# Performance work log

Measured on AMD Instinct MI355X. Metric: run time of the kernel, lower is better.

## Reference

```python
import jax, jax.numpy as jnp
import numpy as np

B, T, C = 2, 2048, 2048
HK, HV, DK, DV, KW = 16, 32, 128, 128, 4
KEY_DIM = HK * DK          # 2048
VAL_DIM = HV * DV          # 4096
QKV_DIM = 2 * KEY_DIM + VAL_DIM  # 8192
REPEAT = HV // HK
EPS = 1e-6


def setup_inputs() -> dict:
    key = jax.random.key(0)
    ks = jax.random.split(key, 12)
    s = 0.02
    return {
        "x": jax.random.normal(ks[0], (B, T, C), jnp.float32),
        "positions": jnp.arange(B * T, dtype=jnp.int64).reshape(B, T) % T,
        "W_qkv": jax.random.normal(ks[1], (QKV_DIM, C), jnp.float32) * s,
        "W_z": jax.random.normal(ks[2], (VAL_DIM, C), jnp.float32) * s,
        "W_b": jax.random.normal(ks[3], (HV, C), jnp.float32) * s,
        "W_a": jax.random.normal(ks[4], (HV, C), jnp.float32) * s,
        "conv_w": jax.random.normal(ks[5], (QKV_DIM, 1, KW), jnp.float32) * 0.3,
        "dt_bias": jnp.ones((HV,), jnp.float32),
        "A_log": jnp.log(jax.random.uniform(ks[6], (HV,), jnp.float32, 0.01, 16.0)),
        "norm_w": jnp.ones((DV,), jnp.float32),
        "W_out": jax.random.normal(ks[7], (C, VAL_DIM), jnp.float32) * s,
    }


def _forward(x, W_qkv, W_z, W_b, W_a, conv_w, dt_bias, A_log, norm_w, W_out):
    qkv = x @ W_qkv.T                                # [B,T,QKV_DIM]
    z = (x @ W_z.T).reshape(B, T, HV, DV)
    b = x @ W_b.T                                    # [B,T,HV]
    a = x @ W_a.T                                    # [B,T,HV]

    # depthwise causal conv1d (left pad KW-1), then SiLU
    qkv_c = jnp.transpose(qkv, (0, 2, 1))            # [B,QKV_DIM,T]
    qkv_c = jax.lax.conv_general_dilated(
        qkv_c, conv_w, window_strides=(1,), padding=[(KW - 1, 0)],
        dimension_numbers=("NCH", "OIH", "NCH"), feature_group_count=QKV_DIM)
    qkv = jax.nn.silu(jnp.transpose(qkv_c, (0, 2, 1)))

    q, k, v = jnp.split(qkv, [KEY_DIM, 2 * KEY_DIM], axis=-1)
    q = q.reshape(B, T, HK, DK)
    k = k.reshape(B, T, HK, DK)
    v = v.reshape(B, T, HV, DV)
    q = q / jnp.maximum(jnp.linalg.norm(q, axis=-1, keepdims=True), 1e-12)
    k = k / jnp.maximum(jnp.linalg.norm(k, axis=-1, keepdims=True), 1e-12)
    if REPEAT > 1:
        q = jnp.repeat(q, REPEAT, axis=2)            # [B,T,HV,DK]
        k = jnp.repeat(k, REPEAT, axis=2)

    beta = jax.nn.sigmoid(b)                         # [B,T,HV]
    g = -jnp.exp(A_log) * jax.nn.softplus(a + dt_bias)  # [B,T,HV]

    # gated delta-rule recurrence over time (lax.scan, time-major)
    def step(state, inp):
        g_t, beta_t, k_t, v_t, q_t = inp             # [B,HV], [B,HV], [B,HV,DK], [B,HV,DV], [B,HV,DK]
        state = jnp.exp(g_t)[..., None, None] * state \
            + beta_t[..., None, None] * (k_t[..., :, None] * v_t[..., None, :])
        out_t = jnp.einsum("bhk,bhkv->bhv", q_t, state)
        return state, out_t

    tm = lambda u: jnp.moveaxis(u, 1, 0)
    state0 = jnp.zeros((B, HV, DK, DV), x.dtype)
    _, out = jax.lax.scan(step, state0, (tm(g), tm(beta), tm(k), tm(v), tm(q)))
    out = jnp.moveaxis(out, 0, 1)                    # [B,T,HV,DV]

    # gated RMSNorm per head: RMSNorm(out) * silu(z)
    o = out.astype(jnp.float32)
    o = o * jax.lax.rsqrt(jnp.mean(o * o, axis=-1, keepdims=True) + EPS)
    o = (norm_w * o) * jax.nn.silu(z.astype(jnp.float32))
    o = o.astype(x.dtype).reshape(B, T, VAL_DIM)
    return o @ W_out.T                               # [B,T,C]


def reference(x, positions, W_qkv, W_z, W_b, W_a, conv_w, dt_bias, A_log, norm_w, W_out):
    del positions  # unused by the module's math
    return _forward(x, W_qkv, W_z, W_b, W_a, conv_w, dt_bias, A_log, norm_w, W_out)
```

## Files before the change

### kernel.cpp

```cpp
#include <hip/hip_runtime.h>

typedef unsigned short u16;
typedef unsigned int u32;
typedef __attribute__((ext_vector_type(8))) short short8;
typedef __attribute__((ext_vector_type(8))) _Float16 half8;
typedef __attribute__((ext_vector_type(4))) float f32x4;

#define NB 2
#define NT 2048
#define NC 2048
#define NHV 32
#define VALD 4096
#define NBT 4096
#define CL 64
#define NCH (NT / CL)

#define GL16(gp, lp) __builtin_amdgcn_global_load_lds( \
    (const __attribute__((address_space(1))) unsigned int*)(gp), \
    (__attribute__((address_space(3))) unsigned int*)(lp), 16, 0, 0)

static __device__ __forceinline__ float bf2f(u16 u) {
  union { u32 u; float f; } x; x.u = ((u32)u) << 16; return x.f;
}
static __device__ __forceinline__ u16 f2bf(float f) {
  union { float f; u32 u; } x; x.f = f;
  u32 r = x.u + 0x7fffu + ((x.u >> 16) & 1u);
  return (u16)(r >> 16);
}
static __device__ __forceinline__ u16 f2h(float f) {
  union { _Float16 h; u16 u; } c; c.h = (_Float16)f; return c.u;
}
static __device__ __forceinline__ float h2f(u16 u) {
  union { u16 u; _Float16 h; } c; c.u = u; return (float)c.h;
}
static __device__ __forceinline__ float sigm(float x) { return 1.0f / (1.0f + __expf(-x)); }
static __device__ __forceinline__ int ldsoff(int row, int c8) {
  return row * 48 + ((c8 ^ ((row >> 2) & 3)) << 3);
}

__global__ void k_sentinel(float* out) { out[0] = 1.0e6f; }

__global__ __launch_bounds__(256) void k_cvtx(const float* __restrict__ in, u16* __restrict__ hi,
                                              u16* __restrict__ lo, u16* __restrict__ h16, int n4) {
  int i = blockIdx.x * 256 + threadIdx.x;
  if (i >= n4) return;
  float4 v = ((const float4*)in)[i];
  ushort4 h, l, p;
  h.x = f2bf(v.x); l.x = f2bf(v.x - bf2f(h.x)); p.x = f2h(v.x);
  h.y = f2bf(v.y); l.y = f2bf(v.y - bf2f(h.y)); p.y = f2h(v.y);
  h.z = f2bf(v.z); l.z = f2bf(v.z - bf2f(h.z)); p.z = f2h(v.z);
  h.w = f2bf(v.w); l.w = f2bf(v.w - bf2f(h.w)); p.w = f2h(v.w);
  ((ushort4*)hi)[i] = h;
  ((ushort4*)lo)[i] = l;
  ((ushort4*)h16)[i] = p;
}

__global__ __launch_bounds__(256) void k_cvt16(const float* __restrict__ in, u16* __restrict__ out, int n4) {
  int i = blockIdx.x * 256 + threadIdx.x;
  if (i >= n4) return;
  float4 v = ((const float4*)in)[i];
  ushort4 o;
  o.x = f2h(v.x); o.y = f2h(v.y); o.z = f2h(v.z); o.w = f2h(v.w);
  ((ushort4*)out)[i] = o;
}

__global__ __launch_bounds__(256) void k_wba(const float* __restrict__ Wb, const float* __restrict__ Wa,
                                             u16* __restrict__ hi, u16* __restrict__ lo) {
  int i = blockIdx.x * 256 + threadIdx.x;
  int r = i >> 11, c = i & 2047;
  float v = 0.f;
  if (r < 32) v = Wb[r * 2048 + c];
  else if (r < 64) v = Wa[(r - 32) * 2048 + c];
  u16 h = f2bf(v);
  hi[i] = h;
  lo[i] = f2bf(v - bf2f(h));
}

__global__ __launch_bounds__(256) void k_gemm_bf3(const u16* __restrict__ Ahg, const u16* __restrict__ Alg,
                                                  const u16* __restrict__ Bhg, const u16* __restrict__ Blg,
                                                  float* __restrict__ C0, int M, int N, int K) {
  __shared__ __align__(16) u16 As_h[128 * 48];
  __shared__ __align__(16) u16 As_l[128 * 48];
  __shared__ __align__(16) u16 Bs_h[128 * 48];
  __shared__ __align__(16) u16 Bs_l[128 * 48];
  const int tid = threadIdx.x;
  const int lane = tid & 63, wave = tid >> 6;
  const int wr = wave >> 1, wc = wave & 1;
  const int l15 = lane & 15, l16 = lane >> 4;
  const int row0 = blockIdx.y * 128, col0 = blockIdx.x * 128;
  const int sr = tid >> 1, sk = (tid & 1) * 16;
  const int c0 = sk >> 3;
  const int w0 = ldsoff(sr, c0), w1 = ldsoff(sr, c0 + 1);
  f32x4 acc[4][4] = {};
  for (int k0 = 0; k0 < K; k0 += 32) {
    const size_t aoff = (size_t)(row0 + sr) * K + k0 + sk;
    const size_t boff = (size_t)(col0 + sr) * K + k0 + sk;
    *(short8*)&As_h[w0] = *(const short8*)&Ahg[aoff];
    *(short8*)&As_h[w1] = *(const short8*)&Ahg[aoff + 8];
    *(short8*)&As_l[w0] = *(const short8*)&Alg[aoff];
    *(short8*)&As_l[w1] = *(const short8*)&Alg[aoff + 8];
    *(short8*)&Bs_h[w0] = *(const short8*)&Bhg[boff];
    *(short8*)&Bs_h[w1] = *(const short8*)&Bhg[boff + 8];
    *(short8*)&Bs_l[w0] = *(const short8*)&Blg[boff];
    *(short8*)&Bs_l[w1] = *(const short8*)&Blg[boff + 8];
    __syncthreads();
    short8 ah[4], al[4], bh[4], bl[4];
#pragma unroll
    for (int mi = 0; mi < 4; ++mi) {
      int off = ldsoff(wr * 64 + mi * 16 + l15, l16);
      ah[mi] = *(short8*)&As_h[off];
      al[mi] = *(short8*)&As_l[off];
    }
#pragma unroll
    for (int ni = 0; ni < 4; ++ni) {
      int off = ldsoff(wc * 64 + ni * 16 + l15, l16);
      bh[ni] = *(short8*)&Bs_h[off];
      bl[ni] = *(short8*)&Bs_l[off];
    }
#pragma unroll
    for (int mi = 0; mi < 4; ++mi)
#pragma unroll
      for (int ni = 0; ni < 4; ++ni) {
        acc[mi][ni] = __builtin_amdgcn_mfma_f32_16x16x32_bf16(ah[mi], bh[ni], acc[mi][ni], 0, 0, 0);
        acc[mi][ni] = __builtin_amdgcn_mfma_f32_16x16x32_bf16(al[mi], bh[ni], acc[mi][ni], 0, 0, 0);
        acc[mi][ni] = __builtin_amdgcn_mfma_f32_16x16x32_bf16(ah[mi], bl[ni], acc[mi][ni], 0, 0, 0);
      }
    __syncthreads();
  }
#pragma unroll
  for (int mi = 0; mi < 4; ++mi)
#pragma unroll
    for (int ni = 0; ni < 4; ++ni) {
      int rr = row0 + wr * 64 + mi * 16 + l16 * 4;
      int cc = col0 + wc * 64 + ni * 16 + l15;
#pragma unroll
      for (int i = 0; i < 4; ++i)
        C0[(size_t)(rr + i) * N + cc] = acc[mi][ni][i];
    }
}

template <int MODE>
__global__ __launch_bounds__(256) void k_gemm16(const u16* __restrict__ Ag, const u16* __restrict__ Bg,
                                                void* __restrict__ C0, int M, int N, int K,
                                                const float* __restrict__ e0, const float* __restrict__ e1,
                                                const float* __restrict__ e2) {
  __shared__ __align__(16) u16 As[128 * 64];
  __shared__ __align__(16) u16 Bs[128 * 64];
  const int tid = threadIdx.x;
  const int lane = tid & 63, wave = tid >> 6;
  const int wr = wave >> 1, wc = wave & 1;
  const int l15 = lane & 15, l16 = lane >> 4;
  const int row0 = blockIdx.y * 128, col0 = blockIdx.x * 128;
  u32 gA[4], gB[4], lofs[4];
#pragma unroll
  for (int i = 0; i < 4; ++i) {
    int o = wave * 2048 + i * 512 + lane * 8;
    int row = o >> 6;
    int cg = ((lane & 7) ^ (row & 7)) * 8;
    gA[i] = (u32)(row0 + row) * (u32)K + cg;
    gB[i] = (u32)(col0 + row) * (u32)K + cg;
    lofs[i] = (u32)(wave * 2048 + i * 512);
  }
  f32x4 acc[4][4] = {};
  for (int k0 = 0; k0 < K; k0 += 64) {
#pragma unroll
    for (int i = 0; i < 4; ++i) {
      GL16(Ag + gA[i] + k0, &As[lofs[i]]);
      GL16(Bg + gB[i] + k0, &Bs[lofs[i]]);
    }
    __syncthreads();
#pragma unroll
    for (int kk = 0; kk < 2; ++kk) {
      half8 a[4], b[4];
#pragma unroll
      for (int mi = 0; mi < 4; ++mi) {
        int row = wr * 64 + mi * 16 + l15;
        a[mi] = *(half8*)&As[row * 64 + (((kk * 4 + l16) ^ (l15 & 7)) << 3)];
      }
#pragma unroll
      for (int ni = 0; ni < 4; ++ni) {
        int row = wc * 64 + ni * 16 + l15;
        b[ni] = *(half8*)&Bs[row * 64 + (((kk * 4 + l16) ^ (l15 & 7)) << 3)];
      }
#pragma unroll
      for (int mi = 0; mi < 4; ++mi)
#pragma unroll
        for (int ni = 0; ni < 4; ++ni)
          acc[mi][ni] = __builtin_amdgcn_mfma_f32_16x16x32_f16(a[mi], b[ni], acc[mi][ni], 0, 0, 0);
    }
    __syncthreads();
  }
#pragma unroll
  for (int mi = 0; mi < 4; ++mi) {
#pragma unroll
    for (int ni = 0; ni < 4; ++ni) {
      int rr = row0 + wr * 64 + mi * 16 + l16 * 4;
      int cc = col0 + wc * 64 + ni * 16 + l15;
#pragma unroll
      for (int i = 0; i < 4; ++i) {
        float v = acc[mi][ni][i];
        size_t idx = (size_t)(rr + i) * N + cc;
        if constexpr (MODE == 0) {
          ((float*)C0)[idx] = v;
        } else if constexpr (MODE == 1) {
          ((u16*)C0)[idx] = f2h(v);
        } else {
          float zs = v * sigm(v);
          float o = e0[idx] * e1[(size_t)(rr + i) * 32 + (cc >> 7)] * e2[cc & 127] * zs;
          ((u16*)C0)[idx] = f2h(o);
        }
      }
    }
  }
}

__global__ __launch_bounds__(256) void k_bg(const float* __restrict__ ba, const float* __restrict__ dt_bias,
                                            const float* __restrict__ A_log, float* __restrict__ beta_t,
                                            float* __restrict__ g_t) {
  int i = blockIdx.x * 256 + threadIdx.x;
  int bt = i >> 5, h = i & 31;
  float bv = ba[(size_t)bt * 128 + h];
  float av = ba[(size_t)bt * 128 + 32 + h];
  beta_t[h * 4096 + bt] = sigm(bv);
  float xx = av + dt_bias[h];
  float sp = (xx > 20.f) ? xx : log1pf(__expf(xx));
  g_t[h * 4096 + bt] = -__expf(A_log[h]) * sp;
}

__global__ __launch_bounds__(256) void k_convqk(const u16* __restrict__ qkraw, const float* __restrict__ cw,
                                                u16* __restrict__ qkn) {
  __shared__ float sval[4096];
  __shared__ float snrm[32];
  const int tid = threadIdx.x;
  const int bt = blockIdx.x;
  const int b = bt >> 11, t = bt & 2047;
  for (int i = 0; i < 16; ++i) {
    int c = i * 256 + tid;
    float acc = 0.f;
#pragma unroll
    for (int j = 0; j < 4; ++j) {
      int ts = t - 3 + j;
      if (ts >= 0) acc += cw[c * 4 + j] * h2f(qkraw[(size_t)(b * 2048 + ts) * 4096 + c]);
    }
    sval[c] = acc * sigm(acc);
  }
  __syncthreads();
  {
    int gidx = tid >> 3, s = tid & 7;
    float ss = 0.f;
#pragma unroll
    for (int i2 = 0; i2 < 16; ++i2) { float v = sval[gidx * 128 + s * 16 + i2]; ss += v * v; }
    ss += __shfl_xor(ss, 1); ss += __shfl_xor(ss, 2); ss += __shfl_xor(ss, 4);
    if (s == 0) snrm[gidx] = 1.0f / fmaxf(sqrtf(ss), 1e-12f);
  }
  __syncthreads();
  for (int i = 0; i < 16; ++i) {
    int c = i * 256 + tid;
    qkn[(size_t)bt * 4096 + c] = f2h(sval[c] * snrm[c >> 7]);
  }
}

__global__ __launch_bounds__(512, 4) void k_scanc(const u16* __restrict__ qk16, const u16* __restrict__ v16,
                                                  const float* __restrict__ cw,
                                                  const float* __restrict__ beta_t, const float* __restrict__ g_t,
                                                  float* __restrict__ outr) {
  __shared__ __align__(16) u16 Qs[64][136], Ks[64][136];
  __shared__ __align__(16) u16 Vs[32][72];
  __shared__ __align__(16) u16 SIs[64][72];
  __shared__ __align__(16) u16 SH[2][32][132];
  __shared__ u16 rv16[67][36];
  __shared__ float garr[64], barr[64], warr[64], earr[64];
  __shared__ float sdt;

  const int tid = threadIdx.x;
  const int lane = tid & 63, wv = tid >> 6;
  const int l15 = lane & 15, l16 = lane >> 4;
  const int dq = blockIdx.x & 3, h = (blockIdx.x >> 2) & 31, b = blockIdx.x >> 7;
  const int bT = b * 2048;
  const int hk = h >> 1;
  const int dvl = tid & 31;
  const int vch = h * 128 + dq * 32;
  const float4 cwv = *(const float4*)&cw[(4096 + vch + dvl) * 4];
  const int mblk = wv & 3, nh = wv >> 2;
  const int m0 = mblk * 16;
  const int sr = tid >> 3, d0 = (tid & 7) * 16;
  const int r0v = tid >> 5;

  for (int i = tid; i < 2 * 32 * 132; i += 512) ((u16*)SH)[i] = 0;
  f32x4 st[2] = {};

  short8 pq[2], pk[2];
  u16 pv[5];
  auto LOADQK = [&](int t0) {
    const size_t base = (size_t)(bT + t0 + sr) * 4096 + hk * 128 + d0;
    pq[0] = *(const short8*)&qk16[base];        pq[1] = *(const short8*)&qk16[base + 8];
    pk[0] = *(const short8*)&qk16[base + 2048]; pk[1] = *(const short8*)&qk16[base + 2056];
  };
  auto LOADV = [&](int t0) {
#pragma unroll
    for (int i = 0; i < 5; ++i) {
      int r = r0v + i * 16;
      int tr = t0 - 3 + r;
      pv[i] = (r < 67 && tr >= 0) ? v16[(size_t)(bT + tr) * 4096 + vch + dvl] : (u16)0;
    }
  };

  LOADQK(0);
  LOADV(0);

  for (int ch = 0; ch < NCH; ++ch) {
    const int t0 = ch * CL;
    const int p = ch & 1;
    *(short8*)&Qs[sr][d0] = pq[0]; *(short8*)&Qs[sr][d0 + 8] = pq[1];
    *(short8*)&Ks[sr][d0] = pk[0]; *(short8*)&Ks[sr][d0 + 8] = pk[1];
#pragma unroll
    for (int i = 0; i < 5; ++i) {
      int r = r0v + i * 16;
      if (r < 67) rv16[r][dvl] = pv[i];
    }
    if (wv == 0) {
      float gv = g_t[h * 4096 + bT + t0 + lane];
      float bv = beta_t[h * 4096 + bT + t0 + lane];
      float cum = gv;
#pragma unroll
      for (int off = 1; off < 64; off <<= 1) {
        float o = __shfl_up(cum, off);
        if (lane >= off) cum += o;
      }
      float tot = __shfl(cum, 63);
      garr[lane] = cum;
      earr[lane] = __expf(cum);
      warr[lane] = __expf(tot - cum) * bv;
      barr[lane] = bv;
      if (lane == 0) sdt = __expf(tot);
    }
    __syncthreads();
    if (ch + 1 < NCH) {
      LOADQK(t0 + CL);
      LOADV(t0 + CL);
    }
    {
      int tl = tid >> 5;
#pragma unroll
      for (int rr = 0; rr < 4; ++rr) {
        int t = rr * 16 + tl;
        float a = cwv.x * h2f(rv16[t][dvl]) + cwv.y * h2f(rv16[t + 1][dvl]) +
                  cwv.z * h2f(rv16[t + 2][dvl]) + cwv.w * h2f(rv16[t + 3][dvl]);
        a = a * sigm(a);
        Vs[dvl][t] = f2h(a);
      }
    }
    half8 a[4];
#pragma unroll
    for (int kk = 0; kk < 4; ++kk) a[kk] = *(half8*)&Qs[m0 + l15][l16 * 8 + kk * 32];
#pragma unroll
    for (int j = 0; j < 2; ++j) {
      int n = nh * 2 + j;
      f32x4 a4 = {};
#pragma unroll
      for (int kk = 0; kk < 4; ++kk) {
        half8 b8 = *(half8*)&Ks[n * 16 + l15][l16 * 8 + kk * 32];
        a4 = __builtin_amdgcn_mfma_f32_16x16x32_f16(a[kk], b8, a4, 0, 0, 0);
      }
      int col = n * 16 + l15;
      float gc = garr[col], bc = barr[col];
#pragma unroll
      for (int i = 0; i < 4; ++i) {
        int row = m0 + l16 * 4 + i;
        float cval = (col <= row) ? __expf(garr[row] - gc) * bc * a4[i] : 0.f;
        SIs[row][col] = f2h(cval);
      }
    }
    __syncthreads();
    f32x4 ao = {};
#pragma unroll
    for (int kk = 0; kk < 4; ++kk) {
      half8 s8 = *(half8*)&SH[p][nh * 16 + l15][l16 * 8 + kk * 32];
      ao = __builtin_amdgcn_mfma_f32_16x16x32_f16(a[kk], s8, ao, 0, 0, 0);
    }
#pragma unroll
    for (int i = 0; i < 4; ++i) ao[i] *= earr[m0 + l16 * 4 + i];
#pragma unroll
    for (int kk = 0; kk < 2; ++kk) {
      half8 asi = *(half8*)&SIs[m0 + l15][l16 * 8 + kk * 32];
      half8 bv8 = *(half8*)&Vs[nh * 16 + l15][l16 * 8 + kk * 32];
      ao = __builtin_amdgcn_mfma_f32_16x16x32_f16(asi, bv8, ao, 0, 0, 0);
    }
#pragma unroll
    for (int i = 0; i < 4; ++i)
      outr[(size_t)(bT + t0 + m0 + l16 * 4 + i) * 4096 + vch + nh * 16 + l15] = ao[i];
#pragma unroll
    for (int m = 0; m < 2; ++m)
#pragma unroll
      for (int i = 0; i < 4; ++i) st[m][i] *= sdt;
#pragma unroll
    for (int kk = 0; kk < 2; ++kk) {
      half8 bw;
      {
        int dk = wv * 16 + l15;
#pragma unroll
        for (int e = 0; e < 8; ++e) {
          int s = l16 * 8 + e + kk * 32;
          bw[e] = (_Float16)(h2f(Ks[s][dk]) * warr[s]);
        }
      }
#pragma unroll
      for (int m = 0; m < 2; ++m) {
        half8 av = *(half8*)&Vs[m * 16 + l15][l16 * 8 + kk * 32];
        st[m] = __builtin_amdgcn_mfma_f32_16x16x32_f16(av, bw, st[m], 0, 0, 0);
      }
    }
#pragma unroll
    for (int m = 0; m < 2; ++m)
#pragma unroll
      for (int i = 0; i < 4; ++i)
        SH[p ^ 1][m * 16 + l16 * 4 + i][wv * 16 + l15] = f2h(st[m][i]);
    __syncthreads();
  }
}

__global__ __launch_bounds__(256) void k_rms(const float* __restrict__ outr, float* __restrict__ rms) {
  int pair = blockIdx.x * 4 + (threadIdx.x >> 6);
  int lane = threadIdx.x & 63;
  float2 v = *(const float2*)&outr[(size_t)pair * 128 + lane * 2];
  float ss = v.x * v.x + v.y * v.y;
#pragma unroll
  for (int m = 1; m < 64; m <<= 1) ss += __shfl_xor(ss, m);
  if (lane == 0) rms[pair] = rsqrtf(ss * (1.0f / 128.0f) + 1e-6f);
}

extern "C" void kernel_launch(void* const* d_in, const int* in_sizes, int n_in,
                              void* d_out, int out_size, void* d_ws, size_t ws_size,
                              hipStream_t stream) {
  const float* x = (const float*)d_in[0];
  const float* W_qkv = (const float*)d_in[2];
  const float* W_z = (const float*)d_in[3];
  const float* W_b = (const float*)d_in[4];
  const float* W_a = (const float*)d_in[5];
  const float* conv_w = (const float*)d_in[6];
  const float* dt_bias = (const float*)d_in[7];
  const float* A_log = (const float*)d_in[8];
  const float* norm_w = (const float*)d_in[9];
  const float* W_out = (const float*)d_in[10];
  float* out = (float*)d_out;

  const size_t MB = 1ull << 20;
  const size_t need = 192 * MB + 3 * (size_t)NBT * 32 * 4;
  if (ws_size < need) {
    k_sentinel<<<1, 1, 0, stream>>>(out);
    return;
  }
  char* ws = (char*)d_ws;
  u16* xh = (u16*)ws;
  u16* xl = (u16*)(ws + 16 * MB);
  u16* xh16 = (u16*)(ws + 32 * MB);
  float* outr = (float*)ws;
  u16* wout16 = (u16*)ws;
  u16* wbah = (u16*)(ws + 64 * MB);
  u16* wbal = (u16*)(ws + 64 * MB + 512 * 1024);
  float* babuf = (float*)(ws + 65 * MB);
  u16* qkB16 = (u16*)(ws + 64 * MB);
  u16* qkA16 = (u16*)(ws + 96 * MB);
  u16* om16 = (u16*)(ws + 96 * MB);
  u16* wsh16 = (u16*)(ws + 128 * MB);
  u16* v16 = (u16*)(ws + 160 * MB);
  u16* xh16b = (u16*)(ws + 128 * MB);
  u16* wz16 = (u16*)(ws + 144 * MB);
  float* beta_t = (float*)(ws + 192 * MB);
  float* g_t = beta_t + (size_t)NBT * 32;
  float* rmsb = g_t + (size_t)NBT * 32;

  const int N4X = NBT * NC / 4;
  k_cvtx<<<N4X / 256, 256, 0, stream>>>(x, xh, xl, xh16, N4X);
  k_cvt16<<<2 * N4X / 256, 256, 0, stream>>>(W_qkv, wsh16, 2 * N4X);
  k_wba<<<128 * NC / 256, 256, 0, stream>>>(W_b, W_a, wbah, wbal);
  k_gemm_bf3<<<dim3(1, NBT / 128), 256, 0, stream>>>(xh, xl, wbah, wbal, babuf, NBT, 128, NC);
  k_bg<<<NBT * 32 / 256, 256, 0, stream>>>(babuf, dt_bias, A_log, beta_t, g_t);

  k_gemm16<1><<<dim3(4096 / 128, NBT / 128), 256, 0, stream>>>(xh16, wsh16, qkA16, NBT, 4096, NC,
                                                               nullptr, nullptr, nullptr);
  k_convqk<<<NBT, 256, 0, stream>>>(qkA16, conv_w, qkB16);

  k_gemm16<1><<<dim3(4096 / 128, NBT / 128), 256, 0, stream>>>(xh16, wsh16 + (size_t)4096 * NC, v16,
                                                               NBT, 4096, NC, nullptr, nullptr, nullptr);

  k_scanc<<<256, 512, 0, stream>>>(qkB16, v16, conv_w, beta_t, g_t, outr);
  k_rms<<<NBT * NHV / 4, 256, 0, stream>>>(outr, rmsb);

  k_cvt16<<<N4X / 256, 256, 0, stream>>>(x, xh16b, N4X);
  k_cvt16<<<N4X / 256, 256, 0, stream>>>(W_z, wz16, N4X);
  k_gemm16<2><<<dim3(VALD / 128, NBT / 128), 256, 0, stream>>>(xh16b, wz16, om16, NBT, VALD, NC,
                                                               outr, rmsb, norm_w);

  k_cvt16<<<N4X / 256, 256, 0, stream>>>(W_out, wout16, N4X);
  k_gemm16<0><<<dim3(NC / 128, NBT / 128), 256, 0, stream>>>(om16, wout16, out, NBT, NC, VALD,
                                                             nullptr, nullptr, nullptr);
}
```

Before: 709.0 us.

## Double-buffer GEMM LDS tiles, store scan output as fp16, reuse converted x

The fp16 GEMM now uses two LDS buffers and issues the next K-tile's global-to-LDS loads before computing on the current tile, dropping one barrier per iteration so load latency overlaps the MFMA work. The scan writes its output in fp16 rather than fp32, which halves that traffic and the reads in the RMS and gated-GEMM epilogue, at some precision cost. The workspace is reorganised so the fp16 copy of x is kept and reused, which removes a redundant conversion of x, and W_z is converted early. Doubling the LDS use per block may reduce occupancy.

```diff
diff --git a/kernel.cpp b/kernel.cpp
--- a/kernel.cpp
+++ b/kernel.cpp
@@ -142,10 +142,10 @@
 template <int MODE>
 __global__ __launch_bounds__(256) void k_gemm16(const u16* __restrict__ Ag, const u16* __restrict__ Bg,
                                                 void* __restrict__ C0, int M, int N, int K,
-                                                const float* __restrict__ e0, const float* __restrict__ e1,
+                                                const u16* __restrict__ e0, const float* __restrict__ e1,
                                                 const float* __restrict__ e2) {
-  __shared__ __align__(16) u16 As[128 * 64];
-  __shared__ __align__(16) u16 Bs[128 * 64];
+  __shared__ __align__(16) u16 As[2 * 128 * 64];
+  __shared__ __align__(16) u16 Bs[2 * 128 * 64];
   const int tid = threadIdx.x;
   const int lane = tid & 63, wave = tid >> 6;
   const int wr = wave >> 1, wc = wave & 1;
@@ -162,25 +162,36 @@
     lofs[i] = (u32)(wave * 2048 + i * 512);
   }
   f32x4 acc[4][4] = {};
-  for (int k0 = 0; k0 < K; k0 += 64) {
-#pragma unroll
-    for (int i = 0; i < 4; ++i) {
-      GL16(Ag + gA[i] + k0, &As[lofs[i]]);
-      GL16(Bg + gB[i] + k0, &Bs[lofs[i]]);
-    }
+  const int NTILE = K >> 6;
+#pragma unroll
+  for (int i = 0; i < 4; ++i) {
+    GL16(Ag + gA[i], &As[lofs[i]]);
+    GL16(Bg + gB[i], &Bs[lofs[i]]);
+  }
+  for (int t = 0; t < NTILE; ++t) {
+    const u32 cb = (u32)(t & 1) * 8192;
     __syncthreads();
+    if (t + 1 < NTILE) {
+      const u32 nb = cb ^ 8192;
+      const int kn = (t + 1) << 6;
+#pragma unroll
+      for (int i = 0; i < 4; ++i) {
+        GL16(Ag + gA[i] + kn, &As[nb + lofs[i]]);
+        GL16(Bg + gB[i] + kn, &Bs[nb + lofs[i]]);
+      }
+    }
 #pragma unroll
     for (int kk = 0; kk < 2; ++kk) {
       half8 a[4], b[4];
 #pragma unroll
       for (int mi = 0; mi < 4; ++mi) {
         int row = wr * 64 + mi * 16 + l15;
-        a[mi] = *(half8*)&As[row * 64 + (((kk * 4 + l16) ^ (l15 & 7)) << 3)];
+        a[mi] = *(half8*)&As[cb + row * 64 + (((kk * 4 + l16) ^ (l15 & 7)) << 3)];
       }
 #pragma unroll
       for (int ni = 0; ni < 4; ++ni) {
         int row = wc * 64 + ni * 16 + l15;
-        b[ni] = *(half8*)&Bs[row * 64 + (((kk * 4 + l16) ^ (l15 & 7)) << 3)];
+        b[ni] = *(half8*)&Bs[cb + row * 64 + (((kk * 4 + l16) ^ (l15 & 7)) << 3)];
       }
 #pragma unroll
       for (int mi = 0; mi < 4; ++mi)
@@ -188,7 +199,6 @@
         for (int ni = 0; ni < 4; ++ni)
           acc[mi][ni] = __builtin_amdgcn_mfma_f32_16x16x32_f16(a[mi], b[ni], acc[mi][ni], 0, 0, 0);
     }
-    __syncthreads();
   }
 #pragma unroll
   for (int mi = 0; mi < 4; ++mi) {
@@ -206,7 +216,7 @@
           ((u16*)C0)[idx] = f2h(v);
         } else {
           float zs = v * sigm(v);
-          float o = e0[idx] * e1[(size_t)(rr + i) * 32 + (cc >> 7)] * e2[cc & 127] * zs;
+          float o = h2f(e0[idx]) * e1[(size_t)(rr + i) * 32 + (cc >> 7)] * e2[cc & 127] * zs;
           ((u16*)C0)[idx] = f2h(o);
         }
       }
@@ -263,7 +273,7 @@
 __global__ __launch_bounds__(512, 4) void k_scanc(const u16* __restrict__ qk16, const u16* __restrict__ v16,
                                                   const float* __restrict__ cw,
                                                   const float* __restrict__ beta_t, const float* __restrict__ g_t,
-                                                  float* __restrict__ outr) {
+                                                  u16* __restrict__ outr) {
   __shared__ __align__(16) u16 Qs[64][136], Ks[64][136];
   __shared__ __align__(16) u16 Vs[32][72];
   __shared__ __align__(16) u16 SIs[64][72];
@@ -388,7 +398,7 @@
     }
 #pragma unroll
     for (int i = 0; i < 4; ++i)
-      outr[(size_t)(bT + t0 + m0 + l16 * 4 + i) * 4096 + vch + nh * 16 + l15] = ao[i];
+      outr[(size_t)(bT + t0 + m0 + l16 * 4 + i) * 4096 + vch + nh * 16 + l15] = f2h(ao[i]);
 #pragma unroll
     for (int m = 0; m < 2; ++m)
 #pragma unroll
@@ -419,11 +429,12 @@
   }
 }
 
-__global__ __launch_bounds__(256) void k_rms(const float* __restrict__ outr, float* __restrict__ rms) {
+__global__ __launch_bounds__(256) void k_rms(const u16* __restrict__ outr, float* __restrict__ rms) {
   int pair = blockIdx.x * 4 + (threadIdx.x >> 6);
   int lane = threadIdx.x & 63;
-  float2 v = *(const float2*)&outr[(size_t)pair * 128 + lane * 2];
-  float ss = v.x * v.x + v.y * v.y;
+  u32 pv = *(const u32*)&outr[(size_t)pair * 128 + lane * 2];
+  float v0 = h2f((u16)pv), v1 = h2f((u16)(pv >> 16));
+  float ss = v0 * v0 + v1 * v1;
 #pragma unroll
   for (int m = 1; m < 64; m <<= 1) ss += __shfl_xor(ss, m);
   if (lane == 0) rms[pair] = rsqrtf(ss * (1.0f / 128.0f) + 1e-6f);
@@ -454,18 +465,17 @@
   u16* xh = (u16*)ws;
   u16* xl = (u16*)(ws + 16 * MB);
   u16* xh16 = (u16*)(ws + 32 * MB);
-  float* outr = (float*)ws;
-  u16* wout16 = (u16*)ws;
-  u16* wbah = (u16*)(ws + 64 * MB);
-  u16* wbal = (u16*)(ws + 64 * MB + 512 * 1024);
-  float* babuf = (float*)(ws + 65 * MB);
+  u16* wz16 = (u16*)(ws + 48 * MB);
   u16* qkB16 = (u16*)(ws + 64 * MB);
+  u16* wout16 = (u16*)(ws + 64 * MB);
   u16* qkA16 = (u16*)(ws + 96 * MB);
   u16* om16 = (u16*)(ws + 96 * MB);
   u16* wsh16 = (u16*)(ws + 128 * MB);
+  u16* outr16 = (u16*)(ws + 128 * MB);
   u16* v16 = (u16*)(ws + 160 * MB);
-  u16* xh16b = (u16*)(ws + 128 * MB);
-  u16* wz16 = (u16*)(ws + 144 * MB);
+  u16* wbah = (u16*)(ws + 160 * MB);
+  u16* wbal = (u16*)(ws + 160 * MB + 512 * 1024);
+  float* babuf = (float*)(ws + 161 * MB);
   float* beta_t = (float*)(ws + 192 * MB);
   float* g_t = beta_t + (size_t)NBT * 32;
   float* rmsb = g_t + (size_t)NBT * 32;
@@ -473,6 +483,7 @@
   const int N4X = NBT * NC / 4;
   k_cvtx<<<N4X / 256, 256, 0, stream>>>(x, xh, xl, xh16, N4X);
   k_cvt16<<<2 * N4X / 256, 256, 0, stream>>>(W_qkv, wsh16, 2 * N4X);
+  k_cvt16<<<N4X / 256, 256, 0, stream>>>(W_z, wz16, N4X);
   k_wba<<<128 * NC / 256, 256, 0, stream>>>(W_b, W_a, wbah, wbal);
   k_gemm_bf3<<<dim3(1, NBT / 128), 256, 0, stream>>>(xh, xl, wbah, wbal, babuf, NBT, 128, NC);
   k_bg<<<NBT * 32 / 256, 256, 0, stream>>>(babuf, dt_bias, A_log, beta_t, g_t);
@@ -484,13 +495,11 @@
   k_gemm16<1><<<dim3(4096 / 128, NBT / 128), 256, 0, stream>>>(xh16, wsh16 + (size_t)4096 * NC, v16,
                                                                NBT, 4096, NC, nullptr, nullptr, nullptr);
 
-  k_scanc<<<256, 512, 0, stream>>>(qkB16, v16, conv_w, beta_t, g_t, outr);
-  k_rms<<<NBT * NHV / 4, 256, 0, stream>>>(outr, rmsb);
-
-  k_cvt16<<<N4X / 256, 256, 0, stream>>>(x, xh16b, N4X);
-  k_cvt16<<<N4X / 256, 256, 0, stream>>>(W_z, wz16, N4X);
-  k_gemm16<2><<<dim3(VALD / 128, NBT / 128), 256, 0, stream>>>(xh16b, wz16, om16, NBT, VALD, NC,
-                                                               outr, rmsb, norm_w);
+  k_scanc<<<256, 512, 0, stream>>>(qkB16, v16, conv_w, beta_t, g_t, outr16);
+  k_rms<<<NBT * NHV / 4, 256, 0, stream>>>(outr16, rmsb);
+
+  k_gemm16<2><<<dim3(VALD / 128, NBT / 128), 256, 0, stream>>>(xh16, wz16, om16, NBT, VALD, NC,
+                                                               outr16, rmsb, norm_w);
 
   k_cvt16<<<N4X / 256, 256, 0, stream>>>(W_out, wout16, N4X);
   k_gemm16<0><<<dim3(NC / 128, NBT / 128), 256, 0, stream>>>(om16, wout16, out, NBT, NC, VALD,
```

Result: faster. 657.6 us (-7.3%).
